# Kernel tuning notes

Hardware: AMD Instinct MI355X
Metric: run time of the kernel (lower is better)

Reference implementation:

```python
import jax, jax.numpy as jnp
import numpy as np

N_EMBD = 768
N_HEAD = 12
HEAD_DIM = N_EMBD // N_HEAD


def setup_inputs() -> dict:
    key = jax.random.key(0)
    k1, k2, k3 = jax.random.split(key, 3)
    x = jax.random.normal(k1, (2, 2048, N_EMBD), dtype=jnp.float32)
    # Dense kernels (no bias), scaled like Glorot-ish init
    w_qkv = jax.random.normal(k2, (N_EMBD, 3 * N_EMBD), dtype=jnp.float32) * (1.0 / np.sqrt(N_EMBD))
    w_proj = jax.random.normal(k3, (N_EMBD, N_EMBD), dtype=jnp.float32) * (1.0 / np.sqrt(N_EMBD))
    return {"x": x, "w_qkv": w_qkv, "w_proj": w_proj}


def reference(x, w_qkv, w_proj):
    b, t, _ = x.shape
    qkv = x @ w_qkv                                  # [b, t, 3*n_embd]
    q, k, v = jnp.split(qkv, 3, axis=-1)
    def split_heads(z):
        return z.reshape(b, t, N_HEAD, HEAD_DIM).transpose(0, 2, 1, 3)  # [b, h, t, d]
    q, k, v = split_heads(q), split_heads(k), split_heads(v)
    scale = jnp.float32(HEAD_DIM) ** -0.5
    att = jnp.einsum('bhqd,bhkd->bhqk', q, k) * scale  # [b, h, t, t]
    # lower-triangular causal mask, additive -1e9 on masked (future) positions
    mask = jnp.tril(jnp.ones((t, t), dtype=jnp.float32))
    att = att + (1.0 - mask)[None, None, :, :] * jnp.float32(-1e9)
    att = jax.nn.softmax(att, axis=-1)
    out = jnp.einsum('bhqk,bhkd->bhqd', att, v)      # [b, h, t, d]
    out = out.transpose(0, 2, 1, 3).reshape(b, t, N_EMBD)
    return out @ w_proj
```

## Files before the change

### kernel.cpp

```cpp
#include <hip/hip_runtime.h>

#define T_SEQ   2048
#define EMBD    768
#define N_HEAD  12
#define HDIM    64
#define BATCH   2

typedef float f32x4 __attribute__((ext_vector_type(4)));
typedef short bf16x8 __attribute__((ext_vector_type(8)));
typedef unsigned short u16;
typedef unsigned int u32;
typedef u16 u16x4 __attribute__((ext_vector_type(4)));

#define MFMA_BF16(a, b, c) __builtin_amdgcn_mfma_f32_16x16x32_bf16((a), (b), (c), 0, 0, 0)

__device__ __forceinline__ u16 f2bf(float f) {
    union { float f; unsigned u; } v; v.f = f;
    unsigned r = v.u + 0x7fffu + ((v.u >> 16) & 1u);
    return (u16)(r >> 16);
}

__device__ __forceinline__ u32 pack2(float hi, float lo) {
    union { float f; u32 u; } a, b;
    a.f = hi; b.f = lo;
    return __builtin_amdgcn_perm(a.u, b.u, 0x07060302u);
}

__device__ __forceinline__ void gload_lds16(const u16* g, u16* l) {
    __builtin_amdgcn_global_load_lds(
        (const __attribute__((address_space(1))) u32*)g,
        (__attribute__((address_space(3))) u32*)l, 16, 0, 0);
}

__global__ __launch_bounds__(256) void convert_bf16(
    const float* __restrict__ x, u16* __restrict__ y, int n)
{
    const int i = (blockIdx.x * 256 + threadIdx.x) * 8;
    if (i >= n) return;
    const float4 f0 = *(const float4*)&x[i];
    const float4 f1 = *(const float4*)&x[i + 4];
    bf16x8 r;
    r[0] = (short)f2bf(f0.x); r[1] = (short)f2bf(f0.y);
    r[2] = (short)f2bf(f0.z); r[3] = (short)f2bf(f0.w);
    r[4] = (short)f2bf(f1.x); r[5] = (short)f2bf(f1.y);
    r[6] = (short)f2bf(f1.z); r[7] = (short)f2bf(f1.w);
    *(bf16x8*)&y[i] = r;
}

__global__ __launch_bounds__(256) void convert_wT(
    const float* __restrict__ W, u16* __restrict__ Wt, int N)
{
    __shared__ float tile[32][33];
    const int c  = threadIdx.x & 31;
    const int r8 = threadIdx.x >> 5;
    const int n0 = blockIdx.x * 32;
    const int k0 = blockIdx.y * 32;
#pragma unroll
    for (int rr = r8; rr < 32; rr += 8)
        tile[rr][c] = W[(size_t)(k0 + rr) * N + n0 + c];
    __syncthreads();
#pragma unroll
    for (int rr = r8; rr < 32; rr += 8)
        Wt[(size_t)(n0 + rr) * 768 + k0 + c] = f2bf(tile[c][rr]);
}

template <int NCOLS, int SCATTER>
__global__ __launch_bounds__(256, 2) void mfma_gemm(
    const u16* __restrict__ A, const u16* __restrict__ Bt,
    float* __restrict__ C, u16* __restrict__ Qo, u16* __restrict__ Ko,
    u16* __restrict__ Vo)
{
    __shared__ u16 As[128 * 32];
    __shared__ u16 Bs[128 * 32];
    const int tid  = threadIdx.x;
    const int lane = tid & 63, wave = tid >> 6;
    const int l15  = lane & 15, quad = lane >> 4;
    const int wy   = wave >> 1, wx = wave & 1;
    const int row0 = blockIdx.y * 128, col0 = blockIdx.x * 128;

    const int sr = lane >> 2;
    const int sc = lane & 3;
    const int sg = sc ^ (sr & 3) ^ (sr >> 2);
    const u16* gA0 = &A [(size_t)(row0 + wave * 16 + sr) * 768 + sg * 8];
    const u16* gA1 = &A [(size_t)(row0 + 64 + wave * 16 + sr) * 768 + sg * 8];
    const u16* gB0 = &Bt[(size_t)(col0 + wave * 16 + sr) * 768 + sg * 8];
    const u16* gB1 = &Bt[(size_t)(col0 + 64 + wave * 16 + sr) * 768 + sg * 8];
    u16* lA0 = &As[wave * 512];
    u16* lA1 = &As[2048 + wave * 512];
    u16* lB0 = &Bs[wave * 512];
    u16* lB1 = &Bs[2048 + wave * 512];

    const int sw = (l15 & 3) ^ (l15 >> 2);

    f32x4 acc[4][4];
#pragma unroll
    for (int i = 0; i < 4; ++i)
#pragma unroll
        for (int j = 0; j < 4; ++j) acc[i][j] = (f32x4){0.f, 0.f, 0.f, 0.f};

    for (int k0 = 0; k0 < 768; k0 += 32) {
        __syncthreads();
        gload_lds16(gA0 + k0, lA0);
        gload_lds16(gA1 + k0, lA1);
        gload_lds16(gB0 + k0, lB0);
        gload_lds16(gB1 + k0, lB1);
        __syncthreads();
        bf16x8 af[4], bfr[4];
#pragma unroll
        for (int mt = 0; mt < 4; ++mt)
            af[mt] = *(const bf16x8*)&As[(wy * 64 + mt * 16 + l15) * 32 + ((quad ^ sw) * 8)];
#pragma unroll
        for (int nt = 0; nt < 4; ++nt)
            bfr[nt] = *(const bf16x8*)&Bs[(wx * 64 + nt * 16 + l15) * 32 + ((quad ^ sw) * 8)];
#pragma unroll
        for (int mt = 0; mt < 4; ++mt)
#pragma unroll
            for (int nt = 0; nt < 4; ++nt)
                acc[mt][nt] = MFMA_BF16(af[mt], bfr[nt], acc[mt][nt]);
    }

    const float qscale = 0.18033688f;
#pragma unroll
    for (int mt = 0; mt < 4; ++mt) {
#pragma unroll
        for (int nt = 0; nt < 4; ++nt) {
            const int col = col0 + wx * 64 + nt * 16 + l15;
            if (SCATTER) {
                const int which = col / 768;
                const int hh = (col - which * 768) >> 6;
                const int dd = col & 63;
                if (which == 2) {
                    const int row = row0 + wy * 64 + mt * 16 + quad * 4;
                    const int bb = row >> 11, t0 = row & 2047;
                    u16x4 pk;
#pragma unroll
                    for (int r = 0; r < 4; ++r) pk[r] = f2bf(acc[mt][nt][r]);
                    *(u16x4*)&Vo[((size_t)(bb * N_HEAD + hh) * HDIM + dd) * T_SEQ + t0] = pk;
                } else {
                    u16* dst = (which == 0) ? Qo : Ko;
                    const float sc2 = (which == 0) ? qscale : 1.0f;
                    const size_t hb = (size_t)hh * T_SEQ * HDIM + dd;
#pragma unroll
                    for (int r = 0; r < 4; ++r) {
                        const int row = row0 + wy * 64 + mt * 16 + quad * 4 + r;
                        const int bb = row >> 11, tt = row & 2047;
                        dst[(size_t)bb * N_HEAD * T_SEQ * HDIM + hb + (size_t)tt * HDIM] =
                            f2bf(acc[mt][nt][r] * sc2);
                    }
                }
            } else {
#pragma unroll
                for (int r = 0; r < 4; ++r) {
                    const int row = row0 + wy * 64 + mt * 16 + quad * 4 + r;
                    C[(size_t)row * NCOLS + col] = acc[mt][nt][r];
                }
            }
        }
    }
}

__global__ __launch_bounds__(256, 3) void attn_mfma(
    const u16* __restrict__ Q, const u16* __restrict__ K,
    const u16* __restrict__ Vt, u16* __restrict__ Aout)
{
    __shared__ float Comb[5120];
    u16* PsAll = (u16*)Comb;

    const int tid  = threadIdx.x;
    const int lane = tid & 63, wave = tid >> 6;
    const int l15  = lane & 15, quad = lane >> 4;

    const int f  = blockIdx.x;
    const int g  = f >> 3;
    const int bh = (f & 7) * 3 + (g >> 6);
    const int j  = 63 - (g & 63);
    const int b  = bh / N_HEAD, h = bh - b * N_HEAD;
    const int qb = j * 32;
    const int nk = (j >> 1) + 1;
    const size_t base = (size_t)bh * T_SEQ * HDIM;

    bf16x8 qf[2][2];
#pragma unroll
    for (int jq = 0; jq < 2; ++jq)
#pragma unroll
        for (int ks = 0; ks < 2; ++ks)
            qf[jq][ks] = *(const bf16x8*)&Q[base + (size_t)(qb + jq * 16 + l15) * HDIM +
                                            ks * 32 + quad * 8];

    f32x4 o[2][4], l_acc[2];
#pragma unroll
    for (int jq = 0; jq < 2; ++jq) {
        l_acc[jq] = (f32x4){0.f, 0.f, 0.f, 0.f};
#pragma unroll
        for (int nt = 0; nt < 4; ++nt) o[jq][nt] = (f32x4){0.f, 0.f, 0.f, 0.f};
    }

    bf16x8 onesf;
#pragma unroll
    for (int u = 0; u < 8; ++u) onesf[u] = (short)0x3F80;

    u16* myPs = PsAll + wave * 2304;

    for (int kt = wave; kt < nk; kt += 4) {
        const int k0 = kt * 64;

        bf16x8 vf[4][2];
#pragma unroll
        for (int nt = 0; nt < 4; ++nt)
#pragma unroll
            for (int ks = 0; ks < 2; ++ks)
                vf[nt][ks] = *(const bf16x8*)&Vt[base + (size_t)(nt * 16 + l15) * T_SEQ +
                                                 k0 + ks * 32 + quad * 8];

        f32x4 s[4][2];
#pragma unroll
        for (int i = 0; i < 4; ++i)
#pragma unroll
            for (int jq = 0; jq < 2; ++jq) s[i][jq] = (f32x4){0.f, 0.f, 0.f, 0.f};
#pragma unroll
        for (int ks = 0; ks < 2; ++ks) {
            bf16x8 kf[4];
#pragma unroll
            for (int i = 0; i < 4; ++i)
                kf[i] = *(const bf16x8*)&K[base + (size_t)(k0 + i * 16 + l15) * HDIM +
                                           ks * 32 + quad * 8];
#pragma unroll
            for (int i = 0; i < 4; ++i)
#pragma unroll
                for (int jq = 0; jq < 2; ++jq)
                    s[i][jq] = MFMA_BF16(kf[i], qf[jq][ks], s[i][jq]);
        }

        const bool need_mask = (k0 + 63 > qb);
#pragma unroll
        for (int i = 0; i < 4; ++i)
#pragma unroll
            for (int jq = 0; jq < 2; ++jq) {
                float pv[4];
                if (need_mask) {
                    const int q = qb + jq * 16 + l15;
#pragma unroll
                    for (int r = 0; r < 4; ++r) {
                        const int key = k0 + i * 16 + quad * 4 + r;
                        pv[r] = exp2f((key > q) ? -1e30f : s[i][jq][r]);
                    }
                } else {
#pragma unroll
                    for (int r = 0; r < 4; ++r) pv[r] = exp2f(s[i][jq][r]);
                }
                uint2 w;
                w.x = pack2(pv[1], pv[0]);
                w.y = pack2(pv[3], pv[2]);
                *(uint2*)&myPs[(jq * 16 + l15) * 72 + i * 16 + quad * 4] = w;
            }

#pragma unroll
        for (int ks = 0; ks < 2; ++ks) {
            bf16x8 pa[2];
#pragma unroll
            for (int jq = 0; jq < 2; ++jq)
                pa[jq] = *(const bf16x8*)&myPs[(jq * 16 + l15) * 72 + ks * 32 + quad * 8];
#pragma unroll
            for (int jq = 0; jq < 2; ++jq) {
#pragma unroll
                for (int nt = 0; nt < 4; ++nt)
                    o[jq][nt] = MFMA_BF16(pa[jq], vf[nt][ks], o[jq][nt]);
                l_acc[jq] = MFMA_BF16(pa[jq], onesf, l_acc[jq]);
            }
        }
    }

    __syncthreads();
    float* R0 = Comb;
    float* R1 = Comb + 2560;
    if (wave == 1 || wave == 3) {
        float* R = (wave == 1) ? R0 : R1;
#pragma unroll
        for (int jq = 0; jq < 2; ++jq) {
#pragma unroll
            for (int nt = 0; nt < 4; ++nt)
#pragma unroll
                for (int r = 0; r < 4; ++r)
                    R[(jq * 16 + nt * 4 + r) * 64 + lane] = o[jq][nt][r];
#pragma unroll
            for (int r = 0; r < 4; ++r)
                R[(32 + jq * 4 + r) * 64 + lane] = l_acc[jq][r];
        }
    }
    __syncthreads();
    if (wave == 0 || wave == 2) {
        float* R = (wave == 0) ? R0 : R1;
#pragma unroll
        for (int jq = 0; jq < 2; ++jq) {
#pragma unroll
            for (int nt = 0; nt < 4; ++nt)
#pragma unroll
                for (int r = 0; r < 4; ++r)
                    o[jq][nt][r] += R[(jq * 16 + nt * 4 + r) * 64 + lane];
#pragma unroll
            for (int r = 0; r < 4; ++r)
                l_acc[jq][r] += R[(32 + jq * 4 + r) * 64 + lane];
        }
        if (wave == 2) {
#pragma unroll
            for (int jq = 0; jq < 2; ++jq) {
#pragma unroll
                for (int nt = 0; nt < 4; ++nt)
#pragma unroll
                    for (int r = 0; r < 4; ++r)
                        R1[(jq * 16 + nt * 4 + r) * 64 + lane] = o[jq][nt][r];
#pragma unroll
                for (int r = 0; r < 4; ++r)
                    R1[(32 + jq * 4 + r) * 64 + lane] = l_acc[jq][r];
            }
        }
    }
    __syncthreads();
    if (wave == 0) {
#pragma unroll
        for (int jq = 0; jq < 2; ++jq) {
#pragma unroll
            for (int nt = 0; nt < 4; ++nt)
#pragma unroll
                for (int r = 0; r < 4; ++r)
                    o[jq][nt][r] += R1[(jq * 16 + nt * 4 + r) * 64 + lane];
#pragma unroll
            for (int r = 0; r < 4; ++r)
                l_acc[jq][r] += R1[(32 + jq * 4 + r) * 64 + lane];
        }
#pragma unroll
        for (int jq = 0; jq < 2; ++jq) {
            f32x4 inv;
#pragma unroll
            for (int r = 0; r < 4; ++r) inv[r] = 1.0f / l_acc[jq][r];
#pragma unroll
            for (int nt = 0; nt < 4; ++nt) {
                const int d = nt * 16 + l15;
#pragma unroll
                for (int r = 0; r < 4; ++r) {
                    const int q = qb + jq * 16 + quad * 4 + r;
                    Aout[(size_t)(b * T_SEQ + q) * EMBD + h * HDIM + d] =
                        f2bf(o[jq][nt][r] * inv[r]);
                }
            }
        }
    }
}

extern "C" void kernel_launch(void* const* d_in, const int* in_sizes, int n_in,
                              void* d_out, int out_size, void* d_ws, size_t ws_size,
                              hipStream_t stream)
{
    (void)in_sizes; (void)n_in; (void)out_size; (void)ws_size;
    const float* x      = (const float*)d_in[0];
    const float* w_qkv  = (const float*)d_in[1];
    const float* w_proj = (const float*)d_in[2];
    float* out = (float*)d_out;

    u16* ws = (u16*)d_ws;
    const size_t NX  = (size_t)BATCH * T_SEQ * EMBD;
    const size_t NWQ = (size_t)EMBD * 3 * EMBD;
    const size_t NWP = (size_t)EMBD * EMBD;
    const size_t SZ  = (size_t)BATCH * N_HEAD * T_SEQ * HDIM;
    u16* xb     = ws;
    u16* wqkvT  = xb + NX;
    u16* wprojT = wqkvT + NWQ;
    u16* Qb     = wprojT + NWP;
    u16* Kb     = Qb + SZ;
    u16* Vtb    = Kb + SZ;
    u16* Ab     = Vtb + SZ;

    dim3 blk(256);
    convert_bf16<<<dim3((int)(NX / 2048)), blk, 0, stream>>>(x, xb, (int)NX);
    convert_wT<<<dim3(3 * EMBD / 32, EMBD / 32), blk, 0, stream>>>(w_qkv, wqkvT, 3 * EMBD);
    convert_wT<<<dim3(EMBD / 32, EMBD / 32), blk, 0, stream>>>(w_proj, wprojT, EMBD);

    mfma_gemm<3 * EMBD, 1><<<dim3(3 * EMBD / 128, BATCH * T_SEQ / 128), blk, 0, stream>>>(
        xb, wqkvT, nullptr, Qb, Kb, Vtb);

    attn_mfma<<<dim3(64 * N_HEAD * BATCH), blk, 0, stream>>>(Qb, Kb, Vtb, Ab);

    mfma_gemm<EMBD, 0><<<dim3(EMBD / 128, BATCH * T_SEQ / 128), blk, 0, stream>>>(
        Ab, wprojT, out, nullptr, nullptr, nullptr);
}
```

Baseline: 187.0 us.

## Fuse prep kernels, deepen GEMM K-tile, pair causal query blocks in attention

```diff
diff --git a/kernel.cpp b/kernel.cpp
--- a/kernel.cpp
+++ b/kernel.cpp
@@ -32,29 +32,34 @@
         (__attribute__((address_space(3))) u32*)l, 16, 0, 0);
 }
 
-__global__ __launch_bounds__(256) void convert_bf16(
-    const float* __restrict__ x, u16* __restrict__ y, int n)
+__global__ __launch_bounds__(256) void prep_kernel(
+    const float* __restrict__ x, const float* __restrict__ wq,
+    const float* __restrict__ wp, u16* __restrict__ xb,
+    u16* __restrict__ wqT, u16* __restrict__ wpT)
 {
-    const int i = (blockIdx.x * 256 + threadIdx.x) * 8;
-    if (i >= n) return;
-    const float4 f0 = *(const float4*)&x[i];
-    const float4 f1 = *(const float4*)&x[i + 4];
-    bf16x8 r;
-    r[0] = (short)f2bf(f0.x); r[1] = (short)f2bf(f0.y);
-    r[2] = (short)f2bf(f0.z); r[3] = (short)f2bf(f0.w);
-    r[4] = (short)f2bf(f1.x); r[5] = (short)f2bf(f1.y);
-    r[6] = (short)f2bf(f1.z); r[7] = (short)f2bf(f1.w);
-    *(bf16x8*)&y[i] = r;
-}
-
-__global__ __launch_bounds__(256) void convert_wT(
-    const float* __restrict__ W, u16* __restrict__ Wt, int N)
-{
+    const int bid = blockIdx.x;
+    const int tid = threadIdx.x;
+    if (bid < 1536) {
+        const int i = bid * 2048 + tid * 8;
+        const float4 f0 = *(const float4*)&x[i];
+        const float4 f1 = *(const float4*)&x[i + 4];
+        bf16x8 r;
+        r[0] = (short)f2bf(f0.x); r[1] = (short)f2bf(f0.y);
+        r[2] = (short)f2bf(f0.z); r[3] = (short)f2bf(f0.w);
+        r[4] = (short)f2bf(f1.x); r[5] = (short)f2bf(f1.y);
+        r[6] = (short)f2bf(f1.z); r[7] = (short)f2bf(f1.w);
+        *(bf16x8*)&xb[i] = r;
+        return;
+    }
     __shared__ float tile[32][33];
-    const int c  = threadIdx.x & 31;
-    const int r8 = threadIdx.x >> 5;
-    const int n0 = blockIdx.x * 32;
-    const int k0 = blockIdx.y * 32;
+    const float* W; u16* Wt; int N, t;
+    if (bid < 3264) { W = wq; Wt = wqT; N = 2304; t = bid - 1536; }
+    else            { W = wp; Wt = wpT; N = 768;  t = bid - 3264; }
+    const int ntiles = N / 32;
+    const int n0 = (t % ntiles) * 32;
+    const int k0 = (t / ntiles) * 32;
+    const int c  = tid & 31;
+    const int r8 = tid >> 5;
 #pragma unroll
     for (int rr = r8; rr < 32; rr += 8)
         tile[rr][c] = W[(size_t)(k0 + rr) * N + n0 + c];
@@ -70,27 +75,26 @@
     float* __restrict__ C, u16* __restrict__ Qo, u16* __restrict__ Ko,
     u16* __restrict__ Vo)
 {
-    __shared__ u16 As[128 * 32];
-    __shared__ u16 Bs[128 * 32];
+    __shared__ u16 As[128 * 64];
+    __shared__ u16 Bs[128 * 64];
     const int tid  = threadIdx.x;
     const int lane = tid & 63, wave = tid >> 6;
     const int l15  = lane & 15, quad = lane >> 4;
     const int wy   = wave >> 1, wx = wave & 1;
     const int row0 = blockIdx.y * 128, col0 = blockIdx.x * 128;
 
-    const int sr = lane >> 2;
-    const int sc = lane & 3;
-    const int sg = sc ^ (sr & 3) ^ (sr >> 2);
-    const u16* gA0 = &A [(size_t)(row0 + wave * 16 + sr) * 768 + sg * 8];
-    const u16* gA1 = &A [(size_t)(row0 + 64 + wave * 16 + sr) * 768 + sg * 8];
-    const u16* gB0 = &Bt[(size_t)(col0 + wave * 16 + sr) * 768 + sg * 8];
-    const u16* gB1 = &Bt[(size_t)(col0 + 64 + wave * 16 + sr) * 768 + sg * 8];
-    u16* lA0 = &As[wave * 512];
-    u16* lA1 = &As[2048 + wave * 512];
-    u16* lB0 = &Bs[wave * 512];
-    u16* lB1 = &Bs[2048 + wave * 512];
-
-    const int sw = (l15 & 3) ^ (l15 >> 2);
+    const int sr = lane >> 3;
+    const int sc = lane & 7;
+    const int g  = sc ^ sr;
+    const u16* gA[4]; const u16* gB[4]; u16* lA[4]; u16* lB[4];
+#pragma unroll
+    for (int i = 0; i < 4; ++i) {
+        const int rb = (i * 4 + wave) * 8;
+        gA[i] = &A [(size_t)(row0 + rb + sr) * 768 + g * 8];
+        gB[i] = &Bt[(size_t)(col0 + rb + sr) * 768 + g * 8];
+        lA[i] = &As[rb * 64];
+        lB[i] = &Bs[rb * 64];
+    }
 
     f32x4 acc[4][4];
 #pragma unroll
@@ -98,25 +102,32 @@
 #pragma unroll
         for (int j = 0; j < 4; ++j) acc[i][j] = (f32x4){0.f, 0.f, 0.f, 0.f};
 
-    for (int k0 = 0; k0 < 768; k0 += 32) {
+    for (int k0 = 0; k0 < 768; k0 += 64) {
         __syncthreads();
-        gload_lds16(gA0 + k0, lA0);
-        gload_lds16(gA1 + k0, lA1);
-        gload_lds16(gB0 + k0, lB0);
-        gload_lds16(gB1 + k0, lB1);
+#pragma unroll
+        for (int i = 0; i < 4; ++i) gload_lds16(gA[i] + k0, lA[i]);
+#pragma unroll
+        for (int i = 0; i < 4; ++i) gload_lds16(gB[i] + k0, lB[i]);
         __syncthreads();
-        bf16x8 af[4], bfr[4];
-#pragma unroll
-        for (int mt = 0; mt < 4; ++mt)
-            af[mt] = *(const bf16x8*)&As[(wy * 64 + mt * 16 + l15) * 32 + ((quad ^ sw) * 8)];
-#pragma unroll
-        for (int nt = 0; nt < 4; ++nt)
-            bfr[nt] = *(const bf16x8*)&Bs[(wx * 64 + nt * 16 + l15) * 32 + ((quad ^ sw) * 8)];
-#pragma unroll
-        for (int mt = 0; mt < 4; ++mt)
-#pragma unroll
-            for (int nt = 0; nt < 4; ++nt)
-                acc[mt][nt] = MFMA_BF16(af[mt], bfr[nt], acc[mt][nt]);
+        bf16x8 af[4][2], bfr[4][2];
+#pragma unroll
+        for (int ks = 0; ks < 2; ++ks) {
+#pragma unroll
+            for (int mt = 0; mt < 4; ++mt)
+                af[mt][ks] = *(const bf16x8*)&As[(wy * 64 + mt * 16 + l15) * 64 +
+                                                 (((ks * 4 + quad) ^ (l15 & 7)) * 8)];
+#pragma unroll
+            for (int nt = 0; nt < 4; ++nt)
+                bfr[nt][ks] = *(const bf16x8*)&Bs[(wx * 64 + nt * 16 + l15) * 64 +
+                                                  (((ks * 4 + quad) ^ (l15 & 7)) * 8)];
+        }
+#pragma unroll
+        for (int ks = 0; ks < 2; ++ks)
+#pragma unroll
+            for (int mt = 0; mt < 4; ++mt)
+#pragma unroll
+                for (int nt = 0; nt < 4; ++nt)
+                    acc[mt][nt] = MFMA_BF16(af[mt][ks], bfr[nt][ks], acc[mt][nt]);
     }
 
     const float qscale = 0.18033688f;
@@ -170,13 +181,16 @@
     const int lane = tid & 63, wave = tid >> 6;
     const int l15  = lane & 15, quad = lane >> 4;
 
-    const int f  = blockIdx.x;
-    const int g  = f >> 3;
-    const int bh = (f & 7) * 3 + (g >> 6);
-    const int j  = 63 - (g & 63);
-    const int b  = bh / N_HEAD, h = bh - b * N_HEAD;
-    const int qb = j * 32;
-    const int nk = (j >> 1) + 1;
+    const int f    = blockIdx.x;
+    const int slot = f >> 3;
+    const int bh   = (f & 7) * 3 + (slot >> 5);
+    const int p    = slot & 31;
+    const int b    = bh / N_HEAD, h = bh - b * N_HEAD;
+
+    const int j      = (wave < 2) ? (63 - p) : p;
+    const int parity = wave & 1;
+    const int qb     = j * 32;
+    const int nk     = (j >> 1) + 1;
     const size_t base = (size_t)bh * T_SEQ * HDIM;
 
     bf16x8 qf[2][2];
@@ -201,8 +215,27 @@
 
     u16* myPs = PsAll + wave * 2304;
 
-    for (int kt = wave; kt < nk; kt += 4) {
+    for (int kt = parity; kt < nk; kt += 2) {
         const int k0 = kt * 64;
+
+        f32x4 s[4][2];
+#pragma unroll
+        for (int i = 0; i < 4; ++i)
+#pragma unroll
+            for (int jq = 0; jq < 2; ++jq) s[i][jq] = (f32x4){0.f, 0.f, 0.f, 0.f};
+#pragma unroll
+        for (int ks = 0; ks < 2; ++ks) {
+            bf16x8 kf[4];
+#pragma unroll
+            for (int i = 0; i < 4; ++i)
+                kf[i] = *(const bf16x8*)&K[base + (size_t)(k0 + i * 16 + l15) * HDIM +
+                                           ks * 32 + quad * 8];
+#pragma unroll
+            for (int i = 0; i < 4; ++i)
+#pragma unroll
+                for (int jq = 0; jq < 2; ++jq)
+                    s[i][jq] = MFMA_BF16(kf[i], qf[jq][ks], s[i][jq]);
+        }
 
         bf16x8 vf[4][2];
 #pragma unroll
@@ -212,32 +245,12 @@
                 vf[nt][ks] = *(const bf16x8*)&Vt[base + (size_t)(nt * 16 + l15) * T_SEQ +
                                                  k0 + ks * 32 + quad * 8];
 
-        f32x4 s[4][2];
-#pragma unroll
-        for (int i = 0; i < 4; ++i)
-#pragma unroll
-            for (int jq = 0; jq < 2; ++jq) s[i][jq] = (f32x4){0.f, 0.f, 0.f, 0.f};
-#pragma unroll
-        for (int ks = 0; ks < 2; ++ks) {
-            bf16x8 kf[4];
-#pragma unroll
-            for (int i = 0; i < 4; ++i)
-                kf[i] = *(const bf16x8*)&K[base + (size_t)(k0 + i * 16 + l15) * HDIM +
-                                           ks * 32 + quad * 8];
-#pragma unroll
-            for (int i = 0; i < 4; ++i)
-#pragma unroll
-                for (int jq = 0; jq < 2; ++jq)
-                    s[i][jq] = MFMA_BF16(kf[i], qf[jq][ks], s[i][jq]);
-        }
-
-        const bool need_mask = (k0 + 63 > qb);
-#pragma unroll
-        for (int i = 0; i < 4; ++i)
+#pragma unroll
+        for (int i = 0; i < 2; ++i)
 #pragma unroll
             for (int jq = 0; jq < 2; ++jq) {
                 float pv[4];
-                if (need_mask) {
+                if (k0 + i * 16 + 15 > qb + jq * 16) {
                     const int q = qb + jq * 16 + l15;
 #pragma unroll
                     for (int r = 0; r < 4; ++r) {
@@ -254,27 +267,57 @@
                 *(uint2*)&myPs[(jq * 16 + l15) * 72 + i * 16 + quad * 4] = w;
             }
 
-#pragma unroll
-        for (int ks = 0; ks < 2; ++ks) {
-            bf16x8 pa[2];
-#pragma unroll
-            for (int jq = 0; jq < 2; ++jq)
-                pa[jq] = *(const bf16x8*)&myPs[(jq * 16 + l15) * 72 + ks * 32 + quad * 8];
+        bf16x8 pa0[2];
+#pragma unroll
+        for (int jq = 0; jq < 2; ++jq)
+            pa0[jq] = *(const bf16x8*)&myPs[(jq * 16 + l15) * 72 + quad * 8];
+
+#pragma unroll
+        for (int i = 2; i < 4; ++i)
 #pragma unroll
             for (int jq = 0; jq < 2; ++jq) {
-#pragma unroll
-                for (int nt = 0; nt < 4; ++nt)
-                    o[jq][nt] = MFMA_BF16(pa[jq], vf[nt][ks], o[jq][nt]);
-                l_acc[jq] = MFMA_BF16(pa[jq], onesf, l_acc[jq]);
+                float pv[4];
+                if (k0 + i * 16 + 15 > qb + jq * 16) {
+                    const int q = qb + jq * 16 + l15;
+#pragma unroll
+                    for (int r = 0; r < 4; ++r) {
+                        const int key = k0 + i * 16 + quad * 4 + r;
+                        pv[r] = exp2f((key > q) ? -1e30f : s[i][jq][r]);
+                    }
+                } else {
+#pragma unroll
+                    for (int r = 0; r < 4; ++r) pv[r] = exp2f(s[i][jq][r]);
+                }
+                uint2 w;
+                w.x = pack2(pv[1], pv[0]);
+                w.y = pack2(pv[3], pv[2]);
+                *(uint2*)&myPs[(jq * 16 + l15) * 72 + i * 16 + quad * 4] = w;
             }
+
+#pragma unroll
+        for (int jq = 0; jq < 2; ++jq) {
+#pragma unroll
+            for (int nt = 0; nt < 4; ++nt)
+                o[jq][nt] = MFMA_BF16(pa0[jq], vf[nt][0], o[jq][nt]);
+            l_acc[jq] = MFMA_BF16(pa0[jq], onesf, l_acc[jq]);
+        }
+
+        bf16x8 pa1[2];
+#pragma unroll
+        for (int jq = 0; jq < 2; ++jq)
+            pa1[jq] = *(const bf16x8*)&myPs[(jq * 16 + l15) * 72 + 32 + quad * 8];
+#pragma unroll
+        for (int jq = 0; jq < 2; ++jq) {
+#pragma unroll
+            for (int nt = 0; nt < 4; ++nt)
+                o[jq][nt] = MFMA_BF16(pa1[jq], vf[nt][1], o[jq][nt]);
+            l_acc[jq] = MFMA_BF16(pa1[jq], onesf, l_acc[jq]);
         }
     }
 
     __syncthreads();
-    float* R0 = Comb;
-    float* R1 = Comb + 2560;
-    if (wave == 1 || wave == 3) {
-        float* R = (wave == 1) ? R0 : R1;
+    if (parity == 1) {
+        float* R = Comb + (wave >> 1) * 2560;
 #pragma unroll
         for (int jq = 0; jq < 2; ++jq) {
 #pragma unroll
@@ -288,8 +331,8 @@
         }
     }
     __syncthreads();
-    if (wave == 0 || wave == 2) {
-        float* R = (wave == 0) ? R0 : R1;
+    if (parity == 0) {
+        const float* R = Comb + (wave >> 1) * 2560;
 #pragma unroll
         for (int jq = 0; jq < 2; ++jq) {
 #pragma unroll
@@ -300,33 +343,6 @@
 #pragma unroll
             for (int r = 0; r < 4; ++r)
                 l_acc[jq][r] += R[(32 + jq * 4 + r) * 64 + lane];
-        }
-        if (wave == 2) {
-#pragma unroll
-            for (int jq = 0; jq < 2; ++jq) {
-#pragma unroll
-                for (int nt = 0; nt < 4; ++nt)
-#pragma unroll
-                    for (int r = 0; r < 4; ++r)
-                        R1[(jq * 16 + nt * 4 + r) * 64 + lane] = o[jq][nt][r];
-#pragma unroll
-                for (int r = 0; r < 4; ++r)
-                    R1[(32 + jq * 4 + r) * 64 + lane] = l_acc[jq][r];
-            }
-        }
-    }
-    __syncthreads();
-    if (wave == 0) {
-#pragma unroll
-        for (int jq = 0; jq < 2; ++jq) {
-#pragma unroll
-            for (int nt = 0; nt < 4; ++nt)
-#pragma unroll
-                for (int r = 0; r < 4; ++r)
-                    o[jq][nt][r] += R1[(jq * 16 + nt * 4 + r) * 64 + lane];
-#pragma unroll
-            for (int r = 0; r < 4; ++r)
-                l_acc[jq][r] += R1[(32 + jq * 4 + r) * 64 + lane];
         }
 #pragma unroll
         for (int jq = 0; jq < 2; ++jq) {
@@ -371,14 +387,12 @@
     u16* Ab     = Vtb + SZ;
 
     dim3 blk(256);
-    convert_bf16<<<dim3((int)(NX / 2048)), blk, 0, stream>>>(x, xb, (int)NX);
-    convert_wT<<<dim3(3 * EMBD / 32, EMBD / 32), blk, 0, stream>>>(w_qkv, wqkvT, 3 * EMBD);
-    convert_wT<<<dim3(EMBD / 32, EMBD / 32), blk, 0, stream>>>(w_proj, wprojT, EMBD);
+    prep_kernel<<<dim3(3840), blk, 0, stream>>>(x, w_qkv, w_proj, xb, wqkvT, wprojT);
 
     mfma_gemm<3 * EMBD, 1><<<dim3(3 * EMBD / 128, BATCH * T_SEQ / 128), blk, 0, stream>>>(
         xb, wqkvT, nullptr, Qb, Kb, Vtb);
 
-    attn_mfma<<<dim3(64 * N_HEAD * BATCH), blk, 0, stream>>>(Qb, Kb, Vtb, Ab);
+    attn_mfma<<<dim3(32 * N_HEAD * BATCH), blk, 0, stream>>>(Qb, Kb, Vtb, Ab);
 
     mfma_gemm<EMBD, 0><<<dim3(EMBD / 128, BATCH * T_SEQ / 128), blk, 0, stream>>>(
         Ab, wprojT, out, nullptr, nullptr, nullptr);
```

Result: faster. 163.8 us (-12.4%).
